# Optimization experiments

Hardware: AMD Instinct MI355X
Metric: run time of the kernel (lower is better)

## Reference

```python
import jax, jax.numpy as jnp
import numpy as np

N = 4096
IN_F = 256
OUT_F = 64
H = 4
NEG_SLOPE = 0.2


def setup_inputs() -> dict:
    key = jax.random.key(0)
    k1, k2, k3, k4 = jax.random.split(key, 4)
    x = jax.random.normal(k1, (N, IN_F), dtype=jnp.float32)
    adj = jax.random.randint(k2, (N, N), 0, 2).astype(jnp.float32)
    # Xavier-uniform init, matching nn.init.xavier_uniform_
    limW = float(np.sqrt(6.0 / (IN_F + OUT_F)))
    W = jax.random.uniform(k3, (H, IN_F, OUT_F), minval=-limW, maxval=limW, dtype=jnp.float32)
    lima = float(np.sqrt(6.0 / (2 * OUT_F + 1)))
    a = jax.random.uniform(k4, (H, 2 * OUT_F, 1), minval=-lima, maxval=lima, dtype=jnp.float32)
    return {"x": x, "adj": adj, "W": W, "a": a}


def reference(x, adj, W, a):
    # x: [N, in], adj: [N, N], W: [H, in, out], a: [H, 2*out, 1]
    n = x.shape[0]
    h, _, fo = W.shape
    Wh = jnp.einsum('nd,hdo->nho', x, W)  # [N, H, O]
    # Additive score: a^T [Wh_i || Wh_j] = (a_src . Wh_i) + (a_dst . Wh_j)
    a_src = a[:, :fo, 0]   # [H, O]
    a_dst = a[:, fo:, 0]   # [H, O]
    s_i = jnp.einsum('nho,ho->nh', Wh, a_src)  # [N, H]
    s_j = jnp.einsum('nho,ho->nh', Wh, a_dst)  # [N, H]
    e = jax.nn.leaky_relu(s_i[:, None, :] + s_j[None, :, :], NEG_SLOPE)  # [N, N, H]
    # Add self-loops on the diagonal, mask non-edges
    idx = jnp.arange(n)
    adj_sl = adj.at[idx, idx].set(1.0)
    mask = (adj_sl != 0)[:, :, None]  # [N, N, 1]
    e_masked = jnp.where(mask, e, -jnp.inf)
    attention = jax.nn.softmax(e_masked, axis=1)  # softmax over neighbors j
    # (dropout is identity in eval mode)
    h_prime = jnp.einsum('ijh,jho->iho', attention, Wh)  # [N, H, O]
    return h_prime.reshape(n, h * fo)  # concat=True
```

## Files before the change

### kernel.cpp

```cpp
#include <hip/hip_runtime.h>
#include <hip/hip_bf16.h>

typedef float    f32x4 __attribute__((ext_vector_type(4)));
typedef _Float16 f16x8 __attribute__((ext_vector_type(8)));
typedef _Float16 f16x4 __attribute__((ext_vector_type(4)));
typedef __fp16   fp16x2 __attribute__((ext_vector_type(2)));

#define NN 4096
#define INF_ 256
#define OUTF 64
#define NH 4
#define NSPL 8
#define NGRP 128
#define LOG2E 1.4426950408889634f

__device__ __forceinline__ unsigned enc_f32(float f) {
    unsigned u = __float_as_uint(f);
    return (u & 0x80000000u) ? ~u : (u | 0x80000000u);
}
__device__ __forceinline__ float dec_f32(unsigned u) {
    return (u & 0x80000000u) ? __uint_as_float(u ^ 0x80000000u)
                             : __uint_as_float(~u);
}

__global__ __launch_bounds__(256) void kW_tr(const float* __restrict__ W,
                                             _Float16* __restrict__ wBh,
                                             _Float16* __restrict__ wBl,
                                             unsigned* __restrict__ smax)
{
    const int b = blockIdx.x;
    const int h = b >> 3, ks = b & 7;
    const int t = threadIdx.x;
    const int ob = t >> 6, lane = t & 63;
    const int row16 = lane & 15, quad = lane >> 4;

    const float* wp = W + (size_t)h*INF_*OUTF + (ks*32 + quad*8)*OUTF + ob*16 + row16;
    f16x8 vh, vl;
#pragma unroll
    for (int e = 0; e < 8; ++e) {
        float v = wp[e*OUTF];
        _Float16 hi = (_Float16)v;
        vh[e] = hi;
        vl[e] = (_Float16)(v - (float)hi);
    }
    const int idx = ((h*8 + ks)*4 + ob)*64 + lane;
    reinterpret_cast<f16x8*>(wBh)[idx] = vh;
    reinterpret_cast<f16x8*>(wBl)[idx] = vl;

    if (b == 0 && t < NH) smax[t] = 0u;
}

__global__ __launch_bounds__(256) void k01(
    const float* __restrict__ adj, unsigned* __restrict__ pack,
    const float* __restrict__ x, const _Float16* __restrict__ wBh,
    const _Float16* __restrict__ wBl, const float* __restrict__ a,
    _Float16* __restrict__ whB, float* __restrict__ s_src,
    float* __restrict__ s_dst, unsigned* __restrict__ smax)
{
    if (blockIdx.x >= 256) {
        const int r    = blockIdx.x - 256;
        const int w    = threadIdx.x >> 6;
        const int lane = threadIdx.x & 63;
        const float* row = adj + (size_t)r * NN + w * 1024;
#pragma unroll
        for (int i = 0; i < 4; ++i) {
            float a0 = row[i*256 + lane];
            float a1 = row[i*256 +  64 + lane];
            float a2 = row[i*256 + 128 + lane];
            float a3 = row[i*256 + 192 + lane];
            unsigned long long bal[4];
            bal[0] = __ballot(a0 != 0.f);
            bal[1] = __ballot(a1 != 0.f);
            bal[2] = __ballot(a2 != 0.f);
            bal[3] = __ballot(a3 != 0.f);
            if (lane < 2) {
#pragma unroll
                for (int k = 0; k < 4; ++k) {
                    int wi = w*32 + i*8 + k*2 + lane;
                    unsigned v = (unsigned)(bal[k] >> (lane * 32));
                    if (wi == (r >> 5)) v |= 1u << (r & 31);
                    pack[r*128 + wi] = v;
                }
            }
        }
        return;
    }

    const int b = blockIdx.x;
    const int h = b >> 6, rb = b & 63;
    const int w = threadIdx.x >> 6, lane = threadIdx.x & 63;
    const int row16 = lane & 15, quad = lane >> 4;
    const int n0 = rb*64 + w*16;

    f32x4 accA[4], accB[4], accC[4];
#pragma unroll
    for (int ob = 0; ob < 4; ++ob) {
        accA[ob] = (f32x4){0,0,0,0};
        accB[ob] = (f32x4){0,0,0,0};
        accC[ob] = (f32x4){0,0,0,0};
    }

    const float* xp = x + (size_t)(n0 + row16)*INF_ + quad*8;
    const f16x8* WH = reinterpret_cast<const f16x8*>(wBh) + (h*8*4)*64 + lane;
    const f16x8* WL = reinterpret_cast<const f16x8*>(wBl) + (h*8*4)*64 + lane;

#pragma unroll
    for (int ks = 0; ks < 8; ++ks) {
        float4 xv0 = *reinterpret_cast<const float4*>(xp + ks*32);
        float4 xv1 = *reinterpret_cast<const float4*>(xp + ks*32 + 4);
        const float xv[8] = {xv0.x,xv0.y,xv0.z,xv0.w,xv1.x,xv1.y,xv1.z,xv1.w};
        f16x8 Ah, Al;
#pragma unroll
        for (int e = 0; e < 8; ++e) {
            _Float16 hi = (_Float16)xv[e];
            Ah[e] = hi;
            Al[e] = (_Float16)(xv[e] - (float)hi);
        }
#pragma unroll
        for (int ob = 0; ob < 4; ++ob) {
            f16x8 bh = WH[(ks*4 + ob)*64];
            f16x8 bl = WL[(ks*4 + ob)*64];
            accA[ob] = __builtin_amdgcn_mfma_f32_16x16x32_f16(Ah, bh, accA[ob], 0, 0, 0);
            accB[ob] = __builtin_amdgcn_mfma_f32_16x16x32_f16(Al, bh, accB[ob], 0, 0, 0);
            accC[ob] = __builtin_amdgcn_mfma_f32_16x16x32_f16(Ah, bl, accC[ob], 0, 0, 0);
        }
    }

    f32x4 acc[4];
#pragma unroll
    for (int ob = 0; ob < 4; ++ob)
        acc[ob] = accA[ob] + accB[ob] + accC[ob];

    {
        const int jblk = n0 >> 5;
        const int qb   = ((n0 & 16) >> 3) + (quad >> 1);
        const int e0   = (quad & 1) * 4;
#pragma unroll
        for (int ob = 0; ob < 4; ++ob) {
            f16x4 st;
#pragma unroll
            for (int q = 0; q < 4; ++q) st[q] = (_Float16)acc[ob][q];
            const size_t off = (((size_t)(h*NGRP + jblk)*4 + ob)*64 + qb*16 + row16)*8 + e0;
            *reinterpret_cast<f16x4*>(whB + off) = st;
        }
    }

    float asv[4], adv[4];
#pragma unroll
    for (int ob = 0; ob < 4; ++ob) {
        asv[ob] = a[h*128 + ob*16 + row16];
        adv[ob] = a[h*128 + 64 + ob*16 + row16];
    }
    float sq_s[4], sq_d[4];
#pragma unroll
    for (int q = 0; q < 4; ++q) {
        float vs = 0.f, vd = 0.f;
#pragma unroll
        for (int ob = 0; ob < 4; ++ob) {
            vs += acc[ob][q] * asv[ob];
            vd += acc[ob][q] * adv[ob];
        }
#pragma unroll
        for (int m = 1; m <= 8; m <<= 1) {
            vs += __shfl_xor(vs, m);
            vd += __shfl_xor(vd, m);
        }
        sq_s[q] = vs; sq_d[q] = vd;
    }
    if (row16 == 0) {
        float vmax = -3.0e38f;
#pragma unroll
        for (int q = 0; q < 4; ++q) {
            const int n = n0 + quad*4 + q;
            s_src[h*NN + n] = LOG2E * sq_s[q];
            const float sd = LOG2E * sq_d[q];
            s_dst[h*NN + n] = sd;
            vmax = fmaxf(vmax, sd);
        }
        atomicMax(&smax[h], enc_f32(vmax));
    }
}

template <int USE_PART>
__global__ __launch_bounds__(256, 4) void k3_attn(
    const unsigned* __restrict__ pack, const _Float16* __restrict__ whB,
    const float* __restrict__ s_src, const float* __restrict__ s_dst,
    const unsigned* __restrict__ smax_enc,
    float* __restrict__ outp, float* __restrict__ l_ws)
{
    constexpr int STEPS_ = NN / NSPL / 32;

    const int b      = blockIdx.x;
    const int jsplit = b % NSPL;
    const int r2     = b / NSPL;
    const int hh     = r2 & 3;
    const int grp    = r2 >> 2;
    const int w      = threadIdx.x >> 6;
    const int lane   = threadIdx.x & 63;
    const int row16  = lane & 15;
    const int quad   = lane >> 4;
    const int i0     = (grp * 4 + w) * 32;
    const int jb0    = jsplit * (NN / NSPL);
    const int jblk0  = jb0 >> 5;

    const float sm = dec_f32(smax_enc[hh]);
    float A1[2], A2[2];
    const unsigned* prow[2];
#pragma unroll
    for (int f = 0; f < 2; ++f) {
        const int ir = i0 + f*16 + row16;
        const float s_i = s_src[hh*NN + ir];
        const float zb  = s_i + sm;
        const float mb  = fmaxf(zb, 0.2f * zb);
        A1[f] = s_i - mb;
        A2[f] = 0.2f * s_i - mb;
        prow[f] = pack + ir*128 + jblk0;
    }

    f32x4 acc[2][4];
    f32x4 accl[2];
#pragma unroll
    for (int f = 0; f < 2; ++f) {
        accl[f] = (f32x4){0,0,0,0};
#pragma unroll
        for (int ob = 0; ob < 4; ++ob) acc[f][ob] = (f32x4){0,0,0,0};
    }

    f16x8 ones;
#pragma unroll
    for (int e = 0; e < 8; ++e) ones[e] = (_Float16)1.0f;

    const _Float16* bB  = whB + (size_t)(hh*NGRP + jblk0)*2048 + lane*8;
    const float*    sdp = s_dst + hh*NN + jb0 + quad*8;

    f16x8 B0 = *reinterpret_cast<const f16x8*>(bB);
    f16x8 B1 = *reinterpret_cast<const f16x8*>(bB + 512);
    f16x8 B2 = *reinterpret_cast<const f16x8*>(bB + 1024);
    f16x8 B3 = *reinterpret_cast<const f16x8*>(bB + 1536);
    unsigned msk0 = prow[0][0], msk1 = prow[1][0];
    float4 sj0 = *reinterpret_cast<const float4*>(sdp);
    float4 sj1 = *reinterpret_cast<const float4*>(sdp + 4);

    for (int s = 0; s < STEPS_; ++s) {
        const _Float16* bn = bB + (s+1)*2048;
        f16x8 nB0 = *reinterpret_cast<const f16x8*>(bn);
        f16x8 nB1 = *reinterpret_cast<const f16x8*>(bn + 512);
        f16x8 nB2 = *reinterpret_cast<const f16x8*>(bn + 1024);
        f16x8 nB3 = *reinterpret_cast<const f16x8*>(bn + 1536);
        unsigned nmsk0 = prow[0][s+1], nmsk1 = prow[1][s+1];
        float4 nsj0 = *reinterpret_cast<const float4*>(sdp + (s+1)*32);
        float4 nsj1 = *reinterpret_cast<const float4*>(sdp + (s+1)*32 + 4);

        const float sjv[8] = {sj0.x,sj0.y,sj0.z,sj0.w,sj1.x,sj1.y,sj1.z,sj1.w};
        float us[8];
#pragma unroll
        for (int e = 0; e < 8; ++e) us[e] = 0.2f * sjv[e];

        const unsigned mskf[2] = {msk0, msk1};
#pragma unroll
        for (int f = 0; f < 2; ++f) {
            const unsigned mm8 = (mskf[f] >> (quad * 8)) & 0xffu;
            float pe[8];
#pragma unroll
            for (int e = 0; e < 8; ++e) {
                float t1 = A1[f] + sjv[e];
                float t2 = A2[f] + us[e];
                float p  = __builtin_amdgcn_exp2f(fmaxf(t1, t2));
                pe[e] = (mm8 & (1u << e)) ? p : 0.0f;
            }
            union { f16x8 v8; fp16x2 p2[4]; } pa;
#pragma unroll
            for (int e2 = 0; e2 < 4; ++e2)
                pa.p2[e2] = __builtin_amdgcn_cvt_pkrtz(pe[2*e2], pe[2*e2+1]);

            acc[f][0] = __builtin_amdgcn_mfma_f32_16x16x32_f16(pa.v8, B0, acc[f][0], 0, 0, 0);
            acc[f][1] = __builtin_amdgcn_mfma_f32_16x16x32_f16(pa.v8, B1, acc[f][1], 0, 0, 0);
            acc[f][2] = __builtin_amdgcn_mfma_f32_16x16x32_f16(pa.v8, B2, acc[f][2], 0, 0, 0);
            acc[f][3] = __builtin_amdgcn_mfma_f32_16x16x32_f16(pa.v8, B3, acc[f][3], 0, 0, 0);
            accl[f]   = __builtin_amdgcn_mfma_f32_16x16x32_f16(pa.v8, ones, accl[f], 0, 0, 0);
        }

        B0 = nB0; B1 = nB1; B2 = nB2; B3 = nB3;
        msk0 = nmsk0; msk1 = nmsk1;
        sj0 = nsj0; sj1 = nsj1;
    }

#pragma unroll
    for (int f = 0; f < 2; ++f) {
        if (row16 == 0) {
#pragma unroll
            for (int q = 0; q < 4; ++q) {
                const int ir = i0 + f*16 + quad*4 + q;
                if (USE_PART) l_ws[(jsplit*NH + hh)*NN + ir] = accl[f][q];
                else          atomicAdd(&l_ws[hh*NN + ir], accl[f][q]);
            }
        }
    }
    if (USE_PART) {
        float* pw = outp + ((size_t)((jsplit*NH + hh)*NGRP + (i0 >> 5))) * 2048 + lane;
#pragma unroll
        for (int f = 0; f < 2; ++f)
#pragma unroll
            for (int ob = 0; ob < 4; ++ob)
#pragma unroll
                for (int q = 0; q < 4; ++q)
                    pw[((f*4 + ob)*4 + q)*64] = acc[f][ob][q];
    } else {
#pragma unroll
        for (int f = 0; f < 2; ++f)
#pragma unroll
            for (int ob = 0; ob < 4; ++ob)
#pragma unroll
                for (int q = 0; q < 4; ++q) {
                    const int grow = i0 + f*16 + quad*4 + q;
                    const int gcol = hh*OUTF + ob*16 + row16;
                    atomicAdd(&outp[(size_t)grow*256 + gcol], acc[f][ob][q]);
                }
    }
}

__global__ __launch_bounds__(256) void k4_part(const float* __restrict__ part,
                                               const float* __restrict__ l_ws,
                                               float* __restrict__ out)
{
    const int idx = blockIdx.x * 256 + threadIdx.x;
    const int n = idx >> 6, c4 = idx & 63;
    const int h = c4 >> 4, k = c4 & 15;
    const int g = n >> 5, f = (n >> 4) & 1, quad = (n >> 2) & 3, q = n & 3;
    const int ob = k >> 2, lb = quad*16 + (k & 3)*4;

    float L = 0.f;
    f32x4 v = {0,0,0,0};
#pragma unroll
    for (int sp = 0; sp < NSPL; ++sp) {
        L += l_ws[(sp*NH + h)*NN + n];
        const float* p = part + ((size_t)((sp*NH + h)*NGRP + g))*2048
                              + ((f*4 + ob)*4 + q)*64 + lb;
        v += *reinterpret_cast<const f32x4*>(p);
    }
    const float inv = 1.0f / L;
    *reinterpret_cast<f32x4*>(out + (size_t)n*256 + c4*4) = v * inv;
}

__global__ __launch_bounds__(256) void k4_atomic(float* __restrict__ out,
                                                 const float* __restrict__ l_acc)
{
    const int idx = blockIdx.x * 256 + threadIdx.x;
    const int n = idx >> 6, c4 = idx & 63, h = c4 >> 4;
    const float inv = 1.0f / l_acc[h*NN + n];
    f32x4 v = *reinterpret_cast<f32x4*>(out + (size_t)n*256 + c4*4);
    *reinterpret_cast<f32x4*>(out + (size_t)n*256 + c4*4) = v * inv;
}

extern "C" void kernel_launch(void* const* d_in, const int* in_sizes, int n_in,
                              void* d_out, int out_size, void* d_ws, size_t ws_size,
                              hipStream_t stream)
{
    const float* x   = (const float*)d_in[0];
    const float* adj = (const float*)d_in[1];
    const float* W   = (const float*)d_in[2];
    const float* a   = (const float*)d_in[3];
    float* out = (float*)d_out;

    char* ws = (char*)d_ws;
    _Float16* whB  = (_Float16*)ws;
    unsigned* pack = (unsigned*)(ws + (2u<<20));
    _Float16* wBh  = (_Float16*)(ws + (4u<<20));
    _Float16* wBl  = (_Float16*)(ws + (4u<<20) + (128u<<10));
    float* s_src   = (float*)(ws + (4u<<20) + (256u<<10));
    float* s_dst   = (float*)(ws + (4u<<20) + (320u<<10));
    unsigned* smax = (unsigned*)(ws + (4u<<20) + (384u<<10));
    float* l_ws    = (float*)(ws + (4u<<20) + (385u<<10));
    float* part    = (float*)(ws + (4u<<20) + (897u<<10));

    const size_t need = (4u<<20) + (897u<<10) + (size_t)NSPL * NN * 256 * 4;

    kW_tr<<<32, 256, 0, stream>>>(W, wBh, wBl, smax);
    k01  <<<256 + NN, 256, 0, stream>>>(adj, pack, x, wBh, wBl, a,
                                        whB, s_src, s_dst, smax);

    if (ws_size >= need) {
        k3_attn<1><<<1024, 256, 0, stream>>>(pack, whB, s_src, s_dst, smax, part, l_ws);
        k4_part<<<1024, 256, 0, stream>>>(part, l_ws, out);
    } else {
        (void)hipMemsetAsync(d_out, 0, (size_t)out_size * sizeof(float), stream);
        (void)hipMemsetAsync(l_ws, 0, NH * NN * sizeof(float), stream);
        k3_attn<0><<<1024, 256, 0, stream>>>(pack, whB, s_src, s_dst, smax, out, l_ws);
        k4_atomic<<<1024, 256, 0, stream>>>(out, l_ws);
    }
}
```

Baseline: 78.24 us.

## Split Wh GEMM K-dimension across waves with LDS reduction in k01

Result: slower. 79.81 us (+2.0%).

```diff
diff --git a/kernel.cpp b/kernel.cpp
--- a/kernel.cpp
+++ b/kernel.cpp
@@ -57,8 +57,12 @@
     _Float16* __restrict__ whB, float* __restrict__ s_src,
     float* __restrict__ s_dst, unsigned* __restrict__ smax)
 {
-    if (blockIdx.x >= 256) {
-        const int r    = blockIdx.x - 256;
+    __shared__ float red[4][4][64][4];
+    __shared__ float red2_s[4][16];
+    __shared__ float red2_d[4][16];
+
+    if (blockIdx.x >= 1024) {
+        const int r    = blockIdx.x - 1024;
         const int w    = threadIdx.x >> 6;
         const int lane = threadIdx.x & 63;
         const float* row = adj + (size_t)r * NN + w * 1024;
@@ -87,10 +91,10 @@
     }
 
     const int b = blockIdx.x;
-    const int h = b >> 6, rb = b & 63;
+    const int h = b >> 8, rg = b & 255;
+    const int n0 = rg * 16;
     const int w = threadIdx.x >> 6, lane = threadIdx.x & 63;
     const int row16 = lane & 15, quad = lane >> 4;
-    const int n0 = rb*64 + w*16;
 
     f32x4 accA[4], accB[4], accC[4];
 #pragma unroll
@@ -105,7 +109,8 @@
     const f16x8* WL = reinterpret_cast<const f16x8*>(wBl) + (h*8*4)*64 + lane;
 
 #pragma unroll
-    for (int ks = 0; ks < 8; ++ks) {
+    for (int ksl = 0; ksl < 2; ++ksl) {
+        const int ks = w*2 + ksl;
         float4 xv0 = *reinterpret_cast<const float4*>(xp + ks*32);
         float4 xv1 = *reinterpret_cast<const float4*>(xp + ks*32 + 4);
         const float xv[8] = {xv0.x,xv0.y,xv0.z,xv0.w,xv1.x,xv1.y,xv1.z,xv1.w};
@@ -126,58 +131,59 @@
         }
     }
 
-    f32x4 acc[4];
-#pragma unroll
-    for (int ob = 0; ob < 4; ++ob)
-        acc[ob] = accA[ob] + accB[ob] + accC[ob];
+#pragma unroll
+    for (int ob = 0; ob < 4; ++ob) {
+        f32x4 p = accA[ob] + accB[ob] + accC[ob];
+        *reinterpret_cast<f32x4*>(&red[w][ob][lane][0]) = p;
+    }
+    __syncthreads();
+
+    const int myob = w;
+    f32x4 acc = *reinterpret_cast<const f32x4*>(&red[0][myob][lane][0]);
+#pragma unroll
+    for (int ws2 = 1; ws2 < 4; ++ws2)
+        acc += *reinterpret_cast<const f32x4*>(&red[ws2][myob][lane][0]);
 
     {
         const int jblk = n0 >> 5;
         const int qb   = ((n0 & 16) >> 3) + (quad >> 1);
         const int e0   = (quad & 1) * 4;
-#pragma unroll
-        for (int ob = 0; ob < 4; ++ob) {
-            f16x4 st;
-#pragma unroll
-            for (int q = 0; q < 4; ++q) st[q] = (_Float16)acc[ob][q];
-            const size_t off = (((size_t)(h*NGRP + jblk)*4 + ob)*64 + qb*16 + row16)*8 + e0;
-            *reinterpret_cast<f16x4*>(whB + off) = st;
-        }
-    }
-
-    float asv[4], adv[4];
-#pragma unroll
-    for (int ob = 0; ob < 4; ++ob) {
-        asv[ob] = a[h*128 + ob*16 + row16];
-        adv[ob] = a[h*128 + 64 + ob*16 + row16];
-    }
-    float sq_s[4], sq_d[4];
+        f16x4 st;
+#pragma unroll
+        for (int q = 0; q < 4; ++q) st[q] = (_Float16)acc[q];
+        const size_t off = (((size_t)(h*NGRP + jblk)*4 + myob)*64 + qb*16 + row16)*8 + e0;
+        *reinterpret_cast<f16x4*>(whB + off) = st;
+    }
+
+    const float as = a[h*128 + myob*16 + row16];
+    const float ad = a[h*128 + 64 + myob*16 + row16];
 #pragma unroll
     for (int q = 0; q < 4; ++q) {
-        float vs = 0.f, vd = 0.f;
-#pragma unroll
-        for (int ob = 0; ob < 4; ++ob) {
-            vs += acc[ob][q] * asv[ob];
-            vd += acc[ob][q] * adv[ob];
-        }
+        float vs = acc[q] * as;
+        float vd = acc[q] * ad;
 #pragma unroll
         for (int m = 1; m <= 8; m <<= 1) {
             vs += __shfl_xor(vs, m);
             vd += __shfl_xor(vd, m);
         }
-        sq_s[q] = vs; sq_d[q] = vd;
-    }
-    if (row16 == 0) {
-        float vmax = -3.0e38f;
-#pragma unroll
-        for (int q = 0; q < 4; ++q) {
-            const int n = n0 + quad*4 + q;
-            s_src[h*NN + n] = LOG2E * sq_s[q];
-            const float sd = LOG2E * sq_d[q];
-            s_dst[h*NN + n] = sd;
-            vmax = fmaxf(vmax, sd);
-        }
-        atomicMax(&smax[h], enc_f32(vmax));
+        if (row16 == 0) {
+            red2_s[myob][quad*4 + q] = vs;
+            red2_d[myob][quad*4 + q] = vd;
+        }
+    }
+    __syncthreads();
+
+    if (threadIdx.x < 16) {
+        const int r = threadIdx.x;
+        const float vs = red2_s[0][r] + red2_s[1][r] + red2_s[2][r] + red2_s[3][r];
+        const float vd = red2_d[0][r] + red2_d[1][r] + red2_d[2][r] + red2_d[3][r];
+        const float sd = LOG2E * vd;
+        s_src[h*NN + n0 + r] = LOG2E * vs;
+        s_dst[h*NN + n0 + r] = sd;
+        float vmax = sd;
+#pragma unroll
+        for (int m = 1; m <= 8; m <<= 1) vmax = fmaxf(vmax, __shfl_xor(vmax, m));
+        if (r == 0) atomicMax(&smax[h], enc_f32(vmax));
     }
 }
 
@@ -376,8 +382,8 @@
     const size_t need = (4u<<20) + (897u<<10) + (size_t)NSPL * NN * 256 * 4;
 
     kW_tr<<<32, 256, 0, stream>>>(W, wBh, wBl, smax);
-    k01  <<<256 + NN, 256, 0, stream>>>(adj, pack, x, wBh, wBl, a,
-                                        whB, s_src, s_dst, smax);
+    k01  <<<1024 + NN, 256, 0, stream>>>(adj, pack, x, wBh, wBl, a,
+                                         whB, s_src, s_dst, smax);
 
     if (ws_size >= need) {
         k3_attn<1><<<1024, 256, 0, stream>>>(pack, whB, s_src, s_dst, smax, part, l_ws);
```
